# Performance work log

Measured on AMD Instinct MI355X. Metric: run time of the kernel, lower is better.

The kernel has to match this reference:

```python
import jax, jax.numpy as jnp
import numpy as np

B, T, I, H, OUT, L = 256, 1200, 16, 128, 1, 2


def _lstm_layer(x, W_ih, W_hh, b_ih, b_hh):
    # x: [B, T, Din]; W_ih: [4H, Din]; W_hh: [4H, H]
    # Precompute input contribution for all timesteps (one big GEMM),
    # then scan only the recurrent part.
    pre = jnp.einsum('btd,gd->btg', x, W_ih) + b_ih + b_hh  # [B, T, 4H]
    pre = jnp.swapaxes(pre, 0, 1)  # [T, B, 4H]
    h0 = jnp.zeros((x.shape[0], W_hh.shape[1]), dtype=x.dtype)
    c0 = jnp.zeros_like(h0)

    def step(carry, p_t):
        h, c = carry
        g = p_t + h @ W_hh.T  # [B, 4H]
        i, f, gg, o = jnp.split(g, 4, axis=-1)  # torch gate order: i, f, g, o
        i = jax.nn.sigmoid(i)
        f = jax.nn.sigmoid(f)
        gg = jnp.tanh(gg)
        o = jax.nn.sigmoid(o)
        c = f * c + i * gg
        h = o * jnp.tanh(c)
        return (h, c), h

    (_, _), hs = jax.lax.scan(step, (h0, c0), pre)  # hs: [T, B, H]
    return jnp.swapaxes(hs, 0, 1)  # [B, T, H]


def setup_inputs() -> dict:
    key = jax.random.key(0)
    ks = jax.random.split(key, 12)
    s = 0.08  # small init scale to keep gates unsaturated
    inp = {
        'x': jax.random.normal(ks[0], (B, T, I), dtype=jnp.float32),
        'W_ih0': jax.random.normal(ks[1], (4 * H, I), dtype=jnp.float32) * s,
        'W_hh0': jax.random.normal(ks[2], (4 * H, H), dtype=jnp.float32) * s,
        'b_ih0': jax.random.normal(ks[3], (4 * H,), dtype=jnp.float32) * s,
        'b_hh0': jax.random.normal(ks[4], (4 * H,), dtype=jnp.float32) * s,
        'W_ih1': jax.random.normal(ks[5], (4 * H, H), dtype=jnp.float32) * s,
        'W_hh1': jax.random.normal(ks[6], (4 * H, H), dtype=jnp.float32) * s,
        'b_ih1': jax.random.normal(ks[7], (4 * H,), dtype=jnp.float32) * s,
        'b_hh1': jax.random.normal(ks[8], (4 * H,), dtype=jnp.float32) * s,
        'W_lin': jax.random.normal(ks[9], (OUT, H), dtype=jnp.float32) * s,
        'b_lin': jax.random.normal(ks[10], (OUT,), dtype=jnp.float32) * s,
    }
    return inp


def reference(x, W_ih0, W_hh0, b_ih0, b_hh0, W_ih1, W_hh1, b_ih1, b_hh1, W_lin, b_lin):
    h1 = _lstm_layer(x, W_ih0, W_hh0, b_ih0, b_hh0)   # [B, T, H]
    h2 = _lstm_layer(h1, W_ih1, W_hh1, b_ih1, b_hh1)  # [B, T, H]
    out = jax.nn.relu(h2)
    out = jnp.einsum('bth,oh->bto', out, W_lin) + b_lin  # [B, T, OUT]
    return out.reshape(-1, 12)  # [B*T*OUT/12, 12]
```

## Files before the change

### kernel.cpp

```cpp
#include <hip/hip_runtime.h>
#include <hip/hip_fp16.h>

#define B_ 256
#define T_ 1200
#define I_ 16
#define H_ 128

typedef __attribute__((ext_vector_type(2))) _Float16 h2;
typedef __attribute__((ext_vector_type(8))) _Float16 f16x8;

union f16x8u { f16x8 v; h2 h[4]; };

#if __has_builtin(__builtin_amdgcn_fdot2)
__device__ __forceinline__ float fdot2(h2 a, h2 b, float c) {
  return __builtin_amdgcn_fdot2(a, b, c, false);
}
#else
__device__ __forceinline__ float fdot2(h2 a, h2 b, float c) {
  return fmaf((float)a.x, (float)b.x, fmaf((float)a.y, (float)b.y, c));
}
#endif

__device__ __forceinline__ float qsum(float x) {
  x += __int_as_float(__builtin_amdgcn_update_dpp(0, __float_as_int(x), 0xB1, 0xF, 0xF, true));
  x += __int_as_float(__builtin_amdgcn_update_dpp(0, __float_as_int(x), 0x4E, 0xF, 0xF, true));
  return x;
}

__device__ __forceinline__ float wred(float x) {
  x += __int_as_float(__builtin_amdgcn_update_dpp(0, __float_as_int(x), 0x141, 0xF, 0xF, true));
  x += __int_as_float(__builtin_amdgcn_update_dpp(0, __float_as_int(x), 0x140, 0xF, 0xF, true));
  x += __shfl_xor(x, 16);
  x += __shfl_xor(x, 32);
  return x;
}

__device__ __forceinline__ float sigm(float x) {
  return __builtin_amdgcn_rcpf(1.f + __expf(-x));
}
__device__ __forceinline__ float tanh_(float x) {
  return 1.f - 2.f * __builtin_amdgcn_rcpf(1.f + __expf(2.f * x));
}

__global__ __attribute__((amdgpu_waves_per_eu(2, 2)))
__launch_bounds__(512) void lstm_fused(
    const float* __restrict__ xin,
    const float* __restrict__ Wih0, const float* __restrict__ Whh0,
    const float* __restrict__ bih0, const float* __restrict__ bhh0,
    const float* __restrict__ Wih1, const float* __restrict__ Whh1,
    const float* __restrict__ bih1, const float* __restrict__ bhh1,
    const float* __restrict__ Wlin, const float* __restrict__ blin,
    float* __restrict__ out)
{
  __shared__ __align__(16) __half buf0[2][H_];
  __shared__ __align__(16) __half buf1[2][H_];
  __shared__ __align__(16) float red[2][8];

  const int tid = threadIdx.x;
  const int c = tid & 3;
  const int j = tid >> 2;
  const int b = blockIdx.x;
  const int wv = tid >> 6;

  h2 w0[4][16], wi[4][16], wh[4][16];
  h2 wx[4][2];
  float bs0[4], bs1[4];

#pragma unroll
  for (int q = 0; q < 4; ++q) {
    const int g = q * H_ + j;
    const float* p0 = Whh0 + (size_t)g * H_ + c * 32;
    const float* p1 = Wih1 + (size_t)g * H_ + c * 32;
    const float* p2 = Whh1 + (size_t)g * H_ + c * 32;
#pragma unroll
    for (int i = 0; i < 8; ++i) {
      float4 v = *(const float4*)(p0 + 4 * i);
      w0[q][2*i].x   = (_Float16)v.x; w0[q][2*i].y   = (_Float16)v.y;
      w0[q][2*i+1].x = (_Float16)v.z; w0[q][2*i+1].y = (_Float16)v.w;
      v = *(const float4*)(p1 + 4 * i);
      wi[q][2*i].x   = (_Float16)v.x; wi[q][2*i].y   = (_Float16)v.y;
      wi[q][2*i+1].x = (_Float16)v.z; wi[q][2*i+1].y = (_Float16)v.w;
      v = *(const float4*)(p2 + 4 * i);
      wh[q][2*i].x   = (_Float16)v.x; wh[q][2*i].y   = (_Float16)v.y;
      wh[q][2*i+1].x = (_Float16)v.z; wh[q][2*i+1].y = (_Float16)v.w;
    }
    const float4 vx = *(const float4*)(Wih0 + (size_t)g * I_ + 4 * c);
    wx[q][0].x = (_Float16)vx.x; wx[q][0].y = (_Float16)vx.y;
    wx[q][1].x = (_Float16)vx.z; wx[q][1].y = (_Float16)vx.w;
    bs0[q] = bih0[g] + bhh0[g];
    bs1[q] = bih1[g] + bhh1[g];
  }
  const float wl = Wlin[j];
  const float bl = blin[0];

  if (tid < H_) {
    buf0[0][tid] = __float2half(0.f);
    buf1[0][tid] = __float2half(0.f);
  }
  float cst0 = 0.f, cst1 = 0.f;
  const float* xp = xin + (size_t)b * T_ * I_ + 4 * c;
  float* op = out + (size_t)b * T_;
  __syncthreads();

#pragma unroll 2
  for (int t = 0; t < T_; ++t) {
    const int rb = t & 1;
    const float4 xv = *(const float4*)xp; xp += I_;
    float a0 = 0.f, a1 = 0.f, a2 = 0.f, a3 = 0.f;
#pragma unroll
    for (int i = 0; i < 4; ++i) {
      f16x8u u; u.v = *(const f16x8*)(&buf0[rb][c * 32 + i * 8]);
#pragma unroll
      for (int p = 0; p < 4; ++p) {
        const h2 hv = u.h[p];
        a0 = fdot2(w0[0][4 * i + p], hv, a0);
        a1 = fdot2(w0[1][4 * i + p], hv, a1);
        a2 = fdot2(w0[2][4 * i + p], hv, a2);
        a3 = fdot2(w0[3][4 * i + p], hv, a3);
      }
    }
    h2 xa, xb;
    xa.x = (_Float16)xv.x; xa.y = (_Float16)xv.y;
    xb.x = (_Float16)xv.z; xb.y = (_Float16)xv.w;
    a0 = fdot2(wx[0][0], xa, fdot2(wx[0][1], xb, a0));
    a1 = fdot2(wx[1][0], xa, fdot2(wx[1][1], xb, a1));
    a2 = fdot2(wx[2][0], xa, fdot2(wx[2][1], xb, a2));
    a3 = fdot2(wx[3][0], xa, fdot2(wx[3][1], xb, a3));
    {
      const float g0 = qsum(a0) + bs0[0];
      const float g1 = qsum(a1) + bs0[1];
      const float g2 = qsum(a2) + bs0[2];
      const float g3 = qsum(a3) + bs0[3];
      const float ig = sigm(g0), fg = sigm(g1), gg = tanh_(g2), og = sigm(g3);
      cst0 = fg * cst0 + ig * gg;
      const float h0v = og * tanh_(cst0);
      if (c == 0) buf0[rb ^ 1][j] = __float2half(h0v);
    }
    __syncthreads();
    a0 = 0.f; a1 = 0.f; a2 = 0.f; a3 = 0.f;
#pragma unroll
    for (int i = 0; i < 4; ++i) {
      f16x8u u; u.v = *(const f16x8*)(&buf0[rb ^ 1][c * 32 + i * 8]);
#pragma unroll
      for (int p = 0; p < 4; ++p) {
        const h2 hv = u.h[p];
        a0 = fdot2(wi[0][4 * i + p], hv, a0);
        a1 = fdot2(wi[1][4 * i + p], hv, a1);
        a2 = fdot2(wi[2][4 * i + p], hv, a2);
        a3 = fdot2(wi[3][4 * i + p], hv, a3);
      }
    }
#pragma unroll
    for (int i = 0; i < 4; ++i) {
      f16x8u u; u.v = *(const f16x8*)(&buf1[rb][c * 32 + i * 8]);
#pragma unroll
      for (int p = 0; p < 4; ++p) {
        const h2 hv = u.h[p];
        a0 = fdot2(wh[0][4 * i + p], hv, a0);
        a1 = fdot2(wh[1][4 * i + p], hv, a1);
        a2 = fdot2(wh[2][4 * i + p], hv, a2);
        a3 = fdot2(wh[3][4 * i + p], hv, a3);
      }
    }
    const float g0 = qsum(a0) + bs1[0];
    const float g1 = qsum(a1) + bs1[1];
    const float g2 = qsum(a2) + bs1[2];
    const float g3 = qsum(a3) + bs1[3];
    const float ig = sigm(g0), fg = sigm(g1), gg = tanh_(g2), og = sigm(g3);
    cst1 = fg * cst1 + ig * gg;
    const float h1v = og * tanh_(cst1);
    if (c == 0) buf1[rb ^ 1][j] = __float2half(h1v);
    float val = wred(fmaxf(h1v, 0.f) * wl);
    if ((tid & 63) == 0) red[rb][wv] = val;
    __syncthreads();
    if (tid == ((t & 7) << 6)) {
      const float4 r0 = *(const float4*)(&red[rb][0]);
      const float4 r1 = *(const float4*)(&red[rb][4]);
      op[t] = bl + r0.x + r0.y + r0.z + r0.w + r1.x + r1.y + r1.z + r1.w;
    }
  }
}

extern "C" void kernel_launch(void* const* d_in, const int* in_sizes, int n_in,
                              void* d_out, int out_size, void* d_ws, size_t ws_size,
                              hipStream_t stream) {
  lstm_fused<<<B_, 512, 0, stream>>>(
      (const float*)d_in[0],
      (const float*)d_in[1], (const float*)d_in[2],
      (const float*)d_in[3], (const float*)d_in[4],
      (const float*)d_in[5], (const float*)d_in[6],
      (const float*)d_in[7], (const float*)d_in[8],
      (const float*)d_in[9], (const float*)d_in[10],
      (float*)d_out);
}
```

Measured before the change: 1.752 ms.

## Split each hidden unit across 8 lanes with 1024-thread blocks

Doubles the block to 1024 threads so each hidden unit's dot products are split over 8 lanes instead of 4, which halves the per-thread serial fdot2 chain and the register-resident weights per step. The reductions are reworked to match the new lane split. Input weights and biases move from registers into shared memory and are reloaded every timestep, and the biases are stored as fp16. This shortens the per-step critical path in exchange for a deeper cross-lane reduction, more waves synchronising at each barrier, extra LDS traffic and slightly lower bias precision.

```diff
diff --git a/kernel.cpp b/kernel.cpp
--- a/kernel.cpp
+++ b/kernel.cpp
@@ -9,7 +9,7 @@
 typedef __attribute__((ext_vector_type(2))) _Float16 h2;
 typedef __attribute__((ext_vector_type(8))) _Float16 f16x8;
 
-union f16x8u { f16x8 v; h2 h[4]; };
+union f16x8u { f16x8 v; h2 h[4]; _Float16 s[8]; };
 
 #if __has_builtin(__builtin_amdgcn_fdot2)
 __device__ __forceinline__ float fdot2(h2 a, h2 b, float c) {
@@ -21,14 +21,14 @@
 }
 #endif
 
-__device__ __forceinline__ float qsum(float x) {
+__device__ __forceinline__ float qsum8(float x) {
   x += __int_as_float(__builtin_amdgcn_update_dpp(0, __float_as_int(x), 0xB1, 0xF, 0xF, true));
   x += __int_as_float(__builtin_amdgcn_update_dpp(0, __float_as_int(x), 0x4E, 0xF, 0xF, true));
+  x += __int_as_float(__builtin_amdgcn_update_dpp(0, __float_as_int(x), 0x141, 0xF, 0xF, true));
   return x;
 }
 
-__device__ __forceinline__ float wred(float x) {
-  x += __int_as_float(__builtin_amdgcn_update_dpp(0, __float_as_int(x), 0x141, 0xF, 0xF, true));
+__device__ __forceinline__ float ored(float x) {
   x += __int_as_float(__builtin_amdgcn_update_dpp(0, __float_as_int(x), 0x140, 0xF, 0xF, true));
   x += __shfl_xor(x, 16);
   x += __shfl_xor(x, 32);
@@ -42,8 +42,7 @@
   return 1.f - 2.f * __builtin_amdgcn_rcpf(1.f + __expf(2.f * x));
 }
 
-__global__ __attribute__((amdgpu_waves_per_eu(2, 2)))
-__launch_bounds__(512) void lstm_fused(
+__global__ __launch_bounds__(1024, 4) void lstm_fused(
     const float* __restrict__ xin,
     const float* __restrict__ Wih0, const float* __restrict__ Whh0,
     const float* __restrict__ bih0, const float* __restrict__ bhh0,
@@ -54,26 +53,26 @@
 {
   __shared__ __align__(16) __half buf0[2][H_];
   __shared__ __align__(16) __half buf1[2][H_];
-  __shared__ __align__(16) float red[2][8];
+  __shared__ __align__(16) float red[2][16];
+  __shared__ __align__(16) h2 lwx[128][8][4];
+  __shared__ __align__(16) __half lbh[128][8];
 
   const int tid = threadIdx.x;
-  const int c = tid & 3;
-  const int j = tid >> 2;
+  const int c = tid & 7;
+  const int j = tid >> 3;
   const int b = blockIdx.x;
   const int wv = tid >> 6;
 
-  h2 w0[4][16], wi[4][16], wh[4][16];
-  h2 wx[4][2];
-  float bs0[4], bs1[4];
+  h2 w0[4][8], wi[4][8], wh[4][8];
 
 #pragma unroll
   for (int q = 0; q < 4; ++q) {
     const int g = q * H_ + j;
-    const float* p0 = Whh0 + (size_t)g * H_ + c * 32;
-    const float* p1 = Wih1 + (size_t)g * H_ + c * 32;
-    const float* p2 = Whh1 + (size_t)g * H_ + c * 32;
-#pragma unroll
-    for (int i = 0; i < 8; ++i) {
+    const float* p0 = Whh0 + (size_t)g * H_ + c * 16;
+    const float* p1 = Wih1 + (size_t)g * H_ + c * 16;
+    const float* p2 = Whh1 + (size_t)g * H_ + c * 16;
+#pragma unroll
+    for (int i = 0; i < 4; ++i) {
       float4 v = *(const float4*)(p0 + 4 * i);
       w0[q][2*i].x   = (_Float16)v.x; w0[q][2*i].y   = (_Float16)v.y;
       w0[q][2*i+1].x = (_Float16)v.z; w0[q][2*i+1].y = (_Float16)v.w;
@@ -84,32 +83,37 @@
       wh[q][2*i].x   = (_Float16)v.x; wh[q][2*i].y   = (_Float16)v.y;
       wh[q][2*i+1].x = (_Float16)v.z; wh[q][2*i+1].y = (_Float16)v.w;
     }
-    const float4 vx = *(const float4*)(Wih0 + (size_t)g * I_ + 4 * c);
-    wx[q][0].x = (_Float16)vx.x; wx[q][0].y = (_Float16)vx.y;
-    wx[q][1].x = (_Float16)vx.z; wx[q][1].y = (_Float16)vx.w;
-    bs0[q] = bih0[g] + bhh0[g];
-    bs1[q] = bih1[g] + bhh1[g];
+    const float2 vx = *(const float2*)(Wih0 + (size_t)g * I_ + 2 * c);
+    h2 t; t.x = (_Float16)vx.x; t.y = (_Float16)vx.y;
+    lwx[j][c][q] = t;
+  }
+  if (tid < H_) {
+#pragma unroll
+    for (int q = 0; q < 4; ++q) {
+      const int g = q * H_ + tid;
+      lbh[tid][q]     = __float2half(bih0[g] + bhh0[g]);
+      lbh[tid][4 + q] = __float2half(bih1[g] + bhh1[g]);
+    }
+    buf0[0][tid] = __float2half(0.f);
+    buf1[0][tid] = __float2half(0.f);
   }
   const float wl = Wlin[j];
   const float bl = blin[0];
 
-  if (tid < H_) {
-    buf0[0][tid] = __float2half(0.f);
-    buf1[0][tid] = __float2half(0.f);
-  }
   float cst0 = 0.f, cst1 = 0.f;
-  const float* xp = xin + (size_t)b * T_ * I_ + 4 * c;
-  float* op = out + (size_t)b * T_;
+  const float* xp = xin + (size_t)b * T_ * I_ + 2 * c;
   __syncthreads();
 
-#pragma unroll 2
+#pragma unroll 1
   for (int t = 0; t < T_; ++t) {
     const int rb = t & 1;
-    const float4 xv = *(const float4*)xp; xp += I_;
+    const float2 xv = *(const float2*)xp; xp += I_;
+    f16x8u wxu; wxu.v = *(const f16x8*)(&lwx[j][c][0]);
+    f16x8u bu;  bu.v  = *(const f16x8*)(&lbh[j][0]);
     float a0 = 0.f, a1 = 0.f, a2 = 0.f, a3 = 0.f;
 #pragma unroll
-    for (int i = 0; i < 4; ++i) {
-      f16x8u u; u.v = *(const f16x8*)(&buf0[rb][c * 32 + i * 8]);
+    for (int i = 0; i < 2; ++i) {
+      f16x8u u; u.v = *(const f16x8*)(&buf0[rb][c * 16 + i * 8]);
 #pragma unroll
       for (int p = 0; p < 4; ++p) {
         const h2 hv = u.h[p];
@@ -119,18 +123,16 @@
         a3 = fdot2(w0[3][4 * i + p], hv, a3);
       }
     }
-    h2 xa, xb;
-    xa.x = (_Float16)xv.x; xa.y = (_Float16)xv.y;
-    xb.x = (_Float16)xv.z; xb.y = (_Float16)xv.w;
-    a0 = fdot2(wx[0][0], xa, fdot2(wx[0][1], xb, a0));
-    a1 = fdot2(wx[1][0], xa, fdot2(wx[1][1], xb, a1));
-    a2 = fdot2(wx[2][0], xa, fdot2(wx[2][1], xb, a2));
-    a3 = fdot2(wx[3][0], xa, fdot2(wx[3][1], xb, a3));
+    h2 xa; xa.x = (_Float16)xv.x; xa.y = (_Float16)xv.y;
+    a0 = fdot2(wxu.h[0], xa, a0);
+    a1 = fdot2(wxu.h[1], xa, a1);
+    a2 = fdot2(wxu.h[2], xa, a2);
+    a3 = fdot2(wxu.h[3], xa, a3);
     {
-      const float g0 = qsum(a0) + bs0[0];
-      const float g1 = qsum(a1) + bs0[1];
-      const float g2 = qsum(a2) + bs0[2];
-      const float g3 = qsum(a3) + bs0[3];
+      const float g0 = qsum8(a0) + (float)bu.s[0];
+      const float g1 = qsum8(a1) + (float)bu.s[1];
+      const float g2 = qsum8(a2) + (float)bu.s[2];
+      const float g3 = qsum8(a3) + (float)bu.s[3];
       const float ig = sigm(g0), fg = sigm(g1), gg = tanh_(g2), og = sigm(g3);
       cst0 = fg * cst0 + ig * gg;
       const float h0v = og * tanh_(cst0);
@@ -139,8 +141,8 @@
     __syncthreads();
     a0 = 0.f; a1 = 0.f; a2 = 0.f; a3 = 0.f;
 #pragma unroll
-    for (int i = 0; i < 4; ++i) {
-      f16x8u u; u.v = *(const f16x8*)(&buf0[rb ^ 1][c * 32 + i * 8]);
+    for (int i = 0; i < 2; ++i) {
+      f16x8u u; u.v = *(const f16x8*)(&buf0[rb ^ 1][c * 16 + i * 8]);
 #pragma unroll
       for (int p = 0; p < 4; ++p) {
         const h2 hv = u.h[p];
@@ -151,8 +153,8 @@
       }
     }
 #pragma unroll
-    for (int i = 0; i < 4; ++i) {
-      f16x8u u; u.v = *(const f16x8*)(&buf1[rb][c * 32 + i * 8]);
+    for (int i = 0; i < 2; ++i) {
+      f16x8u u; u.v = *(const f16x8*)(&buf1[rb][c * 16 + i * 8]);
 #pragma unroll
       for (int p = 0; p < 4; ++p) {
         const h2 hv = u.h[p];
@@ -162,21 +164,25 @@
         a3 = fdot2(wh[3][4 * i + p], hv, a3);
       }
     }
-    const float g0 = qsum(a0) + bs1[0];
-    const float g1 = qsum(a1) + bs1[1];
-    const float g2 = qsum(a2) + bs1[2];
-    const float g3 = qsum(a3) + bs1[3];
+    const float g0 = qsum8(a0) + (float)bu.s[4];
+    const float g1 = qsum8(a1) + (float)bu.s[5];
+    const float g2 = qsum8(a2) + (float)bu.s[6];
+    const float g3 = qsum8(a3) + (float)bu.s[7];
     const float ig = sigm(g0), fg = sigm(g1), gg = tanh_(g2), og = sigm(g3);
     cst1 = fg * cst1 + ig * gg;
     const float h1v = og * tanh_(cst1);
     if (c == 0) buf1[rb ^ 1][j] = __float2half(h1v);
-    float val = wred(fmaxf(h1v, 0.f) * wl);
+    float val = ored(fmaxf(h1v, 0.f) * wl);
     if ((tid & 63) == 0) red[rb][wv] = val;
     __syncthreads();
-    if (tid == ((t & 7) << 6)) {
+    if (tid == ((t & 15) << 6)) {
       const float4 r0 = *(const float4*)(&red[rb][0]);
       const float4 r1 = *(const float4*)(&red[rb][4]);
-      op[t] = bl + r0.x + r0.y + r0.z + r0.w + r1.x + r1.y + r1.z + r1.w;
+      const float4 r2 = *(const float4*)(&red[rb][8]);
+      const float4 r3 = *(const float4*)(&red[rb][12]);
+      out[(size_t)b * T_ + t] = bl
+          + r0.x + r0.y + r0.z + r0.w + r1.x + r1.y + r1.z + r1.w
+          + r2.x + r2.y + r2.z + r2.w + r3.x + r3.y + r3.z + r3.w;
     }
   }
 }
@@ -184,7 +190,7 @@
 extern "C" void kernel_launch(void* const* d_in, const int* in_sizes, int n_in,
                               void* d_out, int out_size, void* d_ws, size_t ws_size,
                               hipStream_t stream) {
-  lstm_fused<<<B_, 512, 0, stream>>>(
+  lstm_fused<<<B_, 1024, 0, stream>>>(
       (const float*)d_in[0],
       (const float*)d_in[1], (const float*)d_in[2],
       (const float*)d_in[3], (const float*)d_in[4],
```

After: 2.704 ms. 1.54x slower.

## Split fused two-layer LSTM into layer0, input-projection GEMM, and layer1 kernels

Applied to the files above, without the earlier changes.

Replaces the single fused kernel with three launches when workspace is large enough. Layer 0 runs its recurrence with x staged in LDS and writes h0 to workspace as fp16. A separate kernel computes the layer-1 input projection for all timesteps. Layer 1 then runs only its recurrent matvec plus the precomputed term. Each thread now owns one full gate row with a broadcast instead of a 4-way reduction, which shortens the per-step serial chain. The cost is about 400 MB of extra global traffic, a serialized second recurrence, and more fp16 rounding in the intermediates.

```diff
diff --git a/kernel.cpp b/kernel.cpp
--- a/kernel.cpp
+++ b/kernel.cpp
@@ -5,11 +5,12 @@
 #define T_ 1200
 #define I_ 16
 #define H_ 128
+#define G4_ (4 * H_)
 
 typedef __attribute__((ext_vector_type(2))) _Float16 h2;
 typedef __attribute__((ext_vector_type(8))) _Float16 f16x8;
 
-union f16x8u { f16x8 v; h2 h[4]; };
+union f16x8u { f16x8 v; h2 h[4]; _Float16 s[8]; };
 
 #if __has_builtin(__builtin_amdgcn_fdot2)
 __device__ __forceinline__ float fdot2(h2 a, h2 b, float c) {
@@ -21,10 +22,9 @@
 }
 #endif
 
-__device__ __forceinline__ float qsum(float x) {
-  x += __int_as_float(__builtin_amdgcn_update_dpp(0, __float_as_int(x), 0xB1, 0xF, 0xF, true));
-  x += __int_as_float(__builtin_amdgcn_update_dpp(0, __float_as_int(x), 0x4E, 0xF, 0xF, true));
-  return x;
+template <int PAT>
+__device__ __forceinline__ float qbcast(float x) {
+  return __int_as_float(__builtin_amdgcn_update_dpp(0, __float_as_int(x), PAT, 0xF, 0xF, true));
 }
 
 __device__ __forceinline__ float wred(float x) {
@@ -42,8 +42,197 @@
   return 1.f - 2.f * __builtin_amdgcn_rcpf(1.f + __expf(2.f * x));
 }
 
-__global__ __attribute__((amdgpu_waves_per_eu(2, 2)))
-__launch_bounds__(512) void lstm_fused(
+__device__ __forceinline__ void load_row_h2(const float* __restrict__ p, h2* w) {
+#pragma unroll
+  for (int i = 0; i < 32; ++i) {
+    const float4 v = *(const float4*)(p + 4 * i);
+    w[2 * i].x     = (_Float16)v.x; w[2 * i].y     = (_Float16)v.y;
+    w[2 * i + 1].x = (_Float16)v.z; w[2 * i + 1].y = (_Float16)v.w;
+  }
+}
+
+__global__ __launch_bounds__(512, 2) void k1_layer0(
+    const float* __restrict__ xin,
+    const float* __restrict__ Wih0, const float* __restrict__ Whh0,
+    const float* __restrict__ bih0, const float* __restrict__ bhh0,
+    __half* __restrict__ h0ws)
+{
+  __shared__ __align__(16) __half xs[T_ * I_];
+  __shared__ __align__(16) __half hb[2][H_];
+
+  const int tid = threadIdx.x;
+  const int q = tid & 3;
+  const int j = tid >> 2;
+  const int g = q * H_ + j;
+  const int b = blockIdx.x;
+
+  {
+    const float4* xg4 = (const float4*)(xin + (size_t)b * T_ * I_);
+    for (int idx = tid; idx < T_ * I_ / 4; idx += 512) {
+      const float4 v = xg4[idx];
+      xs[4 * idx]     = __float2half(v.x);
+      xs[4 * idx + 1] = __float2half(v.y);
+      xs[4 * idx + 2] = __float2half(v.z);
+      xs[4 * idx + 3] = __float2half(v.w);
+    }
+  }
+
+  h2 wh[64], wx[8];
+  load_row_h2(Whh0 + (size_t)g * H_, wh);
+  {
+    const float* px = Wih0 + (size_t)g * I_;
+#pragma unroll
+    for (int i = 0; i < 4; ++i) {
+      const float4 v = *(const float4*)(px + 4 * i);
+      wx[2 * i].x     = (_Float16)v.x; wx[2 * i].y     = (_Float16)v.y;
+      wx[2 * i + 1].x = (_Float16)v.z; wx[2 * i + 1].y = (_Float16)v.w;
+    }
+  }
+  const float bs = bih0[g] + bhh0[g];
+
+  if (tid < H_) hb[0][tid] = __float2half(0.f);
+  float cst = 0.f;
+  __half* h0o = h0ws + (size_t)b * T_ * H_ + j;
+  __syncthreads();
+
+#pragma unroll 2
+  for (int t = 0; t < T_; ++t) {
+    const int rb = t & 1;
+    float a0 = 0.f, a1 = 0.f, a2 = 0.f, a3 = 0.f;
+#pragma unroll
+    for (int i = 0; i < 16; ++i) {
+      f16x8u u; u.v = *(const f16x8*)(&hb[rb][8 * i]);
+      a0 = fdot2(wh[4 * i],     u.h[0], a0);
+      a1 = fdot2(wh[4 * i + 1], u.h[1], a1);
+      a2 = fdot2(wh[4 * i + 2], u.h[2], a2);
+      a3 = fdot2(wh[4 * i + 3], u.h[3], a3);
+    }
+#pragma unroll
+    for (int m = 0; m < 2; ++m) {
+      f16x8u u; u.v = *(const f16x8*)(&xs[t * I_ + 8 * m]);
+      a0 = fdot2(wx[4 * m],     u.h[0], a0);
+      a1 = fdot2(wx[4 * m + 1], u.h[1], a1);
+      a2 = fdot2(wx[4 * m + 2], u.h[2], a2);
+      a3 = fdot2(wx[4 * m + 3], u.h[3], a3);
+    }
+    const float pre = (a0 + a1) + (a2 + a3) + bs;
+    const float ip = qbcast<0x00>(pre);
+    const float fp = qbcast<0x55>(pre);
+    const float gp = qbcast<0xAA>(pre);
+    const float op = qbcast<0xFF>(pre);
+    const float ig = sigm(ip), fg = sigm(fp), gg = tanh_(gp), og = sigm(op);
+    cst = fg * cst + ig * gg;
+    const float hv = og * tanh_(cst);
+    const __half hh = __float2half(hv);
+    if (q == 0) {
+      hb[rb ^ 1][j] = hh;
+      h0o[(size_t)t * H_] = hh;
+    }
+    __syncthreads();
+  }
+}
+
+__global__ __launch_bounds__(512, 2) void k2_pregemm(
+    const __half* __restrict__ h0ws,
+    const float* __restrict__ Wih1,
+    __half* __restrict__ pre1)
+{
+  const int g = threadIdx.x;
+  const int b = blockIdx.x;
+
+  h2 w[64];
+  load_row_h2(Wih1 + (size_t)g * H_, w);
+
+  const __half* hrow = h0ws + (size_t)b * T_ * H_;
+  __half* pp = pre1 + (size_t)b * T_ * G4_ + g;
+
+#pragma unroll 2
+  for (int t = 0; t < T_; ++t) {
+    const __half* hr = hrow + (size_t)t * H_;
+    float a0 = 0.f, a1 = 0.f, a2 = 0.f, a3 = 0.f;
+#pragma unroll
+    for (int i = 0; i < 16; ++i) {
+      f16x8u u; u.v = *(const f16x8*)(hr + 8 * i);
+      a0 = fdot2(w[4 * i],     u.h[0], a0);
+      a1 = fdot2(w[4 * i + 1], u.h[1], a1);
+      a2 = fdot2(w[4 * i + 2], u.h[2], a2);
+      a3 = fdot2(w[4 * i + 3], u.h[3], a3);
+    }
+    pp[(size_t)t * G4_] = __float2half((a0 + a1) + (a2 + a3));
+  }
+}
+
+__global__ __launch_bounds__(512, 2) void k3_layer1(
+    const __half* __restrict__ pre1,
+    const float* __restrict__ Whh1,
+    const float* __restrict__ bih1, const float* __restrict__ bhh1,
+    const float* __restrict__ Wlin, const float* __restrict__ blin,
+    float* __restrict__ out)
+{
+  __shared__ __align__(16) __half hb[2][H_];
+  __shared__ __align__(16) float red[2][8];
+
+  const int tid = threadIdx.x;
+  const int q = tid & 3;
+  const int j = tid >> 2;
+  const int g = q * H_ + j;
+  const int b = blockIdx.x;
+  const int wv = tid >> 6;
+
+  h2 w[64];
+  load_row_h2(Whh1 + (size_t)g * H_, w);
+  const float bs = bih1[g] + bhh1[g];
+  const float wl = Wlin[j];
+  const float bl = blin[0];
+
+  if (tid < H_) hb[0][tid] = __float2half(0.f);
+  float cst = 0.f;
+  const __half* pp = pre1 + (size_t)b * T_ * G4_ + g;
+  float* op = out + (size_t)b * T_;
+  __syncthreads();
+
+  __half pnext = pp[0];
+#pragma unroll 2
+  for (int t = 0; t < T_; ++t) {
+    const int rb = t & 1;
+    const __half pcur = pnext;
+    if (t + 1 < T_) pnext = pp[(size_t)(t + 1) * G4_];
+    float a0 = 0.f, a1 = 0.f, a2 = 0.f, a3 = 0.f;
+#pragma unroll
+    for (int i = 0; i < 16; ++i) {
+      f16x8u u; u.v = *(const f16x8*)(&hb[rb][8 * i]);
+      a0 = fdot2(w[4 * i],     u.h[0], a0);
+      a1 = fdot2(w[4 * i + 1], u.h[1], a1);
+      a2 = fdot2(w[4 * i + 2], u.h[2], a2);
+      a3 = fdot2(w[4 * i + 3], u.h[3], a3);
+    }
+    const float pre = (a0 + a1) + (a2 + a3) + __half2float(pcur) + bs;
+    const float ip = qbcast<0x00>(pre);
+    const float fp = qbcast<0x55>(pre);
+    const float gp = qbcast<0xAA>(pre);
+    const float op_ = qbcast<0xFF>(pre);
+    const float ig = sigm(ip), fg = sigm(fp), gg = tanh_(gp), og = sigm(op_);
+    cst = fg * cst + ig * gg;
+    const float hv = og * tanh_(cst);
+    if (q == 0) hb[rb ^ 1][j] = __float2half(hv);
+    float val = wred(fmaxf(hv, 0.f) * wl);
+    if ((tid & 63) == 0) red[rb][wv] = val;
+    __syncthreads();
+    if (tid == ((t & 7) << 6)) {
+      const float4 r0 = *(const float4*)(&red[rb][0]);
+      const float4 r1 = *(const float4*)(&red[rb][4]);
+      op[t] = bl + r0.x + r0.y + r0.z + r0.w + r1.x + r1.y + r1.z + r1.w;
+    }
+  }
+}
+
+__device__ __forceinline__ float qsum8f(float x) {
+  x += __int_as_float(__builtin_amdgcn_update_dpp(0, __float_as_int(x), 0xB1, 0xF, 0xF, true));
+  x += __int_as_float(__builtin_amdgcn_update_dpp(0, __float_as_int(x), 0x4E, 0xF, 0xF, true));
+  return x;
+}
+
+__global__ __launch_bounds__(512, 2) void lstm_fused_fb(
     const float* __restrict__ xin,
     const float* __restrict__ Wih0, const float* __restrict__ Whh0,
     const float* __restrict__ bih0, const float* __restrict__ bhh0,
@@ -67,28 +256,28 @@
   float bs0[4], bs1[4];
 
 #pragma unroll
-  for (int q = 0; q < 4; ++q) {
-    const int g = q * H_ + j;
+  for (int qq = 0; qq < 4; ++qq) {
+    const int g = qq * H_ + j;
     const float* p0 = Whh0 + (size_t)g * H_ + c * 32;
     const float* p1 = Wih1 + (size_t)g * H_ + c * 32;
     const float* p2 = Whh1 + (size_t)g * H_ + c * 32;
 #pragma unroll
     for (int i = 0; i < 8; ++i) {
       float4 v = *(const float4*)(p0 + 4 * i);
-      w0[q][2*i].x   = (_Float16)v.x; w0[q][2*i].y   = (_Float16)v.y;
-      w0[q][2*i+1].x = (_Float16)v.z; w0[q][2*i+1].y = (_Float16)v.w;
+      w0[qq][2*i].x   = (_Float16)v.x; w0[qq][2*i].y   = (_Float16)v.y;
+      w0[qq][2*i+1].x = (_Float16)v.z; w0[qq][2*i+1].y = (_Float16)v.w;
       v = *(const float4*)(p1 + 4 * i);
-      wi[q][2*i].x   = (_Float16)v.x; wi[q][2*i].y   = (_Float16)v.y;
-      wi[q][2*i+1].x = (_Float16)v.z; wi[q][2*i+1].y = (_Float16)v.w;
+      wi[qq][2*i].x   = (_Float16)v.x; wi[qq][2*i].y   = (_Float16)v.y;
+      wi[qq][2*i+1].x = (_Float16)v.z; wi[qq][2*i+1].y = (_Float16)v.w;
       v = *(const float4*)(p2 + 4 * i);
-      wh[q][2*i].x   = (_Float16)v.x; wh[q][2*i].y   = (_Float16)v.y;
-      wh[q][2*i+1].x = (_Float16)v.z; wh[q][2*i+1].y = (_Float16)v.w;
+      wh[qq][2*i].x   = (_Float16)v.x; wh[qq][2*i].y   = (_Float16)v.y;
+      wh[qq][2*i+1].x = (_Float16)v.z; wh[qq][2*i+1].y = (_Float16)v.w;
     }
     const float4 vx = *(const float4*)(Wih0 + (size_t)g * I_ + 4 * c);
-    wx[q][0].x = (_Float16)vx.x; wx[q][0].y = (_Float16)vx.y;
-    wx[q][1].x = (_Float16)vx.z; wx[q][1].y = (_Float16)vx.w;
-    bs0[q] = bih0[g] + bhh0[g];
-    bs1[q] = bih1[g] + bhh1[g];
+    wx[qq][0].x = (_Float16)vx.x; wx[qq][0].y = (_Float16)vx.y;
+    wx[qq][1].x = (_Float16)vx.z; wx[qq][1].y = (_Float16)vx.w;
+    bs0[qq] = bih0[g] + bhh0[g];
+    bs1[qq] = bih1[g] + bhh1[g];
   }
   const float wl = Wlin[j];
   const float bl = blin[0];
@@ -127,10 +316,10 @@
     a2 = fdot2(wx[2][0], xa, fdot2(wx[2][1], xb, a2));
     a3 = fdot2(wx[3][0], xa, fdot2(wx[3][1], xb, a3));
     {
-      const float g0 = qsum(a0) + bs0[0];
-      const float g1 = qsum(a1) + bs0[1];
-      const float g2 = qsum(a2) + bs0[2];
-      const float g3 = qsum(a3) + bs0[3];
+      const float g0 = qsum8f(a0) + bs0[0];
+      const float g1 = qsum8f(a1) + bs0[1];
+      const float g2 = qsum8f(a2) + bs0[2];
+      const float g3 = qsum8f(a3) + bs0[3];
       const float ig = sigm(g0), fg = sigm(g1), gg = tanh_(g2), og = sigm(g3);
       cst0 = fg * cst0 + ig * gg;
       const float h0v = og * tanh_(cst0);
@@ -162,10 +351,10 @@
         a3 = fdot2(wh[3][4 * i + p], hv, a3);
       }
     }
-    const float g0 = qsum(a0) + bs1[0];
-    const float g1 = qsum(a1) + bs1[1];
-    const float g2 = qsum(a2) + bs1[2];
-    const float g3 = qsum(a3) + bs1[3];
+    const float g0 = qsum8f(a0) + bs1[0];
+    const float g1 = qsum8f(a1) + bs1[1];
+    const float g2 = qsum8f(a2) + bs1[2];
+    const float g3 = qsum8f(a3) + bs1[3];
     const float ig = sigm(g0), fg = sigm(g1), gg = tanh_(g2), og = sigm(g3);
     cst1 = fg * cst1 + ig * gg;
     const float h1v = og * tanh_(cst1);
@@ -184,12 +373,32 @@
 extern "C" void kernel_launch(void* const* d_in, const int* in_sizes, int n_in,
                               void* d_out, int out_size, void* d_ws, size_t ws_size,
                               hipStream_t stream) {
-  lstm_fused<<<B_, 512, 0, stream>>>(
-      (const float*)d_in[0],
-      (const float*)d_in[1], (const float*)d_in[2],
-      (const float*)d_in[3], (const float*)d_in[4],
-      (const float*)d_in[5], (const float*)d_in[6],
-      (const float*)d_in[7], (const float*)d_in[8],
-      (const float*)d_in[9], (const float*)d_in[10],
-      (float*)d_out);
-}
+  const size_t H0_BYTES  = (size_t)B_ * T_ * H_ * sizeof(__half);
+  const size_t PRE_BYTES = (size_t)B_ * T_ * G4_ * sizeof(__half);
+
+  if (d_ws != nullptr && ws_size >= H0_BYTES + PRE_BYTES) {
+    __half* h0ws = (__half*)d_ws;
+    __half* pre1 = (__half*)((char*)d_ws + H0_BYTES);
+    k1_layer0<<<B_, 512, 0, stream>>>(
+        (const float*)d_in[0],
+        (const float*)d_in[1], (const float*)d_in[2],
+        (const float*)d_in[3], (const float*)d_in[4],
+        h0ws);
+    k2_pregemm<<<B_, 512, 0, stream>>>(
+        h0ws, (const float*)d_in[5], pre1);
+    k3_layer1<<<B_, 512, 0, stream>>>(
+        pre1, (const float*)d_in[6],
+        (const float*)d_in[7], (const float*)d_in[8],
+        (const float*)d_in[9], (const float*)d_in[10],
+        (float*)d_out);
+  } else {
+    lstm_fused_fb<<<B_, 512, 0, stream>>>(
+        (const float*)d_in[0],
+        (const float*)d_in[1], (const float*)d_in[2],
+        (const float*)d_in[3], (const float*)d_in[4],
+        (const float*)d_in[5], (const float*)d_in[6],
+        (const float*)d_in[7], (const float*)d_in[8],
+        (const float*)d_in[9], (const float*)d_in[10],
+        (float*)d_out);
+  }
+}
```

New measurement: 1.751 ms. Within noise of the previous version (-0.1%).

## Pipeline LSTM layers across timesteps with one barrier per step and per-thread gate rows

Applied to the files above, without the earlier changes.

Layer 1 for step t-1 now runs in the same iteration as layer 0 for step t, which cuts the block barriers from two per step to one. Each thread owns a full gate row, so the cross-lane reductions are replaced by one unified sigmoid/tanh activation per lane and DPP broadcasts of the four gates. The input sequence is staged into LDS as fp16 up front, and the output reduction is deferred by a step. In exchange, each thread holds about 200 half2 weight registers, which risks register pressure or spills. Every thread also reads the whole h vector from LDS, which raises LDS traffic.

```diff
diff --git a/kernel.cpp b/kernel.cpp
--- a/kernel.cpp
+++ b/kernel.cpp
@@ -9,7 +9,7 @@
 typedef __attribute__((ext_vector_type(2))) _Float16 h2;
 typedef __attribute__((ext_vector_type(8))) _Float16 f16x8;
 
-union f16x8u { f16x8 v; h2 h[4]; };
+union f16x8u { f16x8 v; h2 h[4]; _Float16 s[8]; };
 
 #if __has_builtin(__builtin_amdgcn_fdot2)
 __device__ __forceinline__ float fdot2(h2 a, h2 b, float c) {
@@ -21,10 +21,9 @@
 }
 #endif
 
-__device__ __forceinline__ float qsum(float x) {
-  x += __int_as_float(__builtin_amdgcn_update_dpp(0, __float_as_int(x), 0xB1, 0xF, 0xF, true));
-  x += __int_as_float(__builtin_amdgcn_update_dpp(0, __float_as_int(x), 0x4E, 0xF, 0xF, true));
-  return x;
+template <int PAT>
+__device__ __forceinline__ float qbcast(float x) {
+  return __int_as_float(__builtin_amdgcn_update_dpp(0, __float_as_int(x), PAT, 0xF, 0xF, true));
 }
 
 __device__ __forceinline__ float wred(float x) {
@@ -35,15 +34,27 @@
   return x;
 }
 
-__device__ __forceinline__ float sigm(float x) {
-  return __builtin_amdgcn_rcpf(1.f + __expf(-x));
-}
 __device__ __forceinline__ float tanh_(float x) {
   return 1.f - 2.f * __builtin_amdgcn_rcpf(1.f + __expf(2.f * x));
 }
 
-__global__ __attribute__((amdgpu_waves_per_eu(2, 2)))
-__launch_bounds__(512) void lstm_fused(
+__device__ __forceinline__ void load_row_h2(const float* __restrict__ p, h2* w) {
+#pragma unroll
+  for (int i = 0; i < 32; ++i) {
+    const float4 v = *(const float4*)(p + 4 * i);
+    w[2 * i].x     = (_Float16)v.x; w[2 * i].y     = (_Float16)v.y;
+    w[2 * i + 1].x = (_Float16)v.z; w[2 * i + 1].y = (_Float16)v.w;
+  }
+}
+
+__device__ __forceinline__ void lds_barrier() {
+  __builtin_amdgcn_sched_barrier(0);
+  asm volatile("s_waitcnt lgkmcnt(0)" ::: "memory");
+  __builtin_amdgcn_s_barrier();
+  __builtin_amdgcn_sched_barrier(0);
+}
+
+__global__ __launch_bounds__(512, 2) void lstm_one(
     const float* __restrict__ xin,
     const float* __restrict__ Wih0, const float* __restrict__ Whh0,
     const float* __restrict__ bih0, const float* __restrict__ bhh0,
@@ -52,139 +63,151 @@
     const float* __restrict__ Wlin, const float* __restrict__ blin,
     float* __restrict__ out)
 {
-  __shared__ __align__(16) __half buf0[2][H_];
-  __shared__ __align__(16) __half buf1[2][H_];
+  __shared__ __align__(16) __half xs[T_ * I_];
+  __shared__ __align__(16) __half h0b[2][H_];
+  __shared__ __align__(16) __half h1b[2][H_];
   __shared__ __align__(16) float red[2][8];
 
   const int tid = threadIdx.x;
-  const int c = tid & 3;
+  const int q = tid & 3;
   const int j = tid >> 2;
+  const int g = q * H_ + j;
   const int b = blockIdx.x;
-  const int wv = tid >> 6;
-
-  h2 w0[4][16], wi[4][16], wh[4][16];
-  h2 wx[4][2];
-  float bs0[4], bs1[4];
-
-#pragma unroll
-  for (int q = 0; q < 4; ++q) {
-    const int g = q * H_ + j;
-    const float* p0 = Whh0 + (size_t)g * H_ + c * 32;
-    const float* p1 = Wih1 + (size_t)g * H_ + c * 32;
-    const float* p2 = Whh1 + (size_t)g * H_ + c * 32;
-#pragma unroll
-    for (int i = 0; i < 8; ++i) {
-      float4 v = *(const float4*)(p0 + 4 * i);
-      w0[q][2*i].x   = (_Float16)v.x; w0[q][2*i].y   = (_Float16)v.y;
-      w0[q][2*i+1].x = (_Float16)v.z; w0[q][2*i+1].y = (_Float16)v.w;
-      v = *(const float4*)(p1 + 4 * i);
-      wi[q][2*i].x   = (_Float16)v.x; wi[q][2*i].y   = (_Float16)v.y;
-      wi[q][2*i+1].x = (_Float16)v.z; wi[q][2*i+1].y = (_Float16)v.w;
-      v = *(const float4*)(p2 + 4 * i);
-      wh[q][2*i].x   = (_Float16)v.x; wh[q][2*i].y   = (_Float16)v.y;
-      wh[q][2*i+1].x = (_Float16)v.z; wh[q][2*i+1].y = (_Float16)v.w;
-    }
-    const float4 vx = *(const float4*)(Wih0 + (size_t)g * I_ + 4 * c);
-    wx[q][0].x = (_Float16)vx.x; wx[q][0].y = (_Float16)vx.y;
-    wx[q][1].x = (_Float16)vx.z; wx[q][1].y = (_Float16)vx.w;
-    bs0[q] = bih0[g] + bhh0[g];
-    bs1[q] = bih1[g] + bhh1[g];
-  }
+
+  {
+    const float4* xg4 = (const float4*)(xin + (size_t)b * T_ * I_);
+    for (int idx = tid; idx < T_ * I_ / 4; idx += 512) {
+      const float4 v = xg4[idx];
+      xs[4 * idx]     = __float2half(v.x);
+      xs[4 * idx + 1] = __float2half(v.y);
+      xs[4 * idx + 2] = __float2half(v.z);
+      xs[4 * idx + 3] = __float2half(v.w);
+    }
+  }
+
+  h2 w0[64], wi[64], w1[64], wx[8];
+  load_row_h2(Whh0 + (size_t)g * H_, w0);
+  load_row_h2(Wih1 + (size_t)g * H_, wi);
+  load_row_h2(Whh1 + (size_t)g * H_, w1);
+  {
+    const float* px = Wih0 + (size_t)g * I_;
+#pragma unroll
+    for (int i = 0; i < 4; ++i) {
+      const float4 v = *(const float4*)(px + 4 * i);
+      wx[2 * i].x     = (_Float16)v.x; wx[2 * i].y     = (_Float16)v.y;
+      wx[2 * i + 1].x = (_Float16)v.z; wx[2 * i + 1].y = (_Float16)v.w;
+    }
+  }
+  const float bs0 = bih0[g] + bhh0[g];
+  const float bs1 = bih1[g] + bhh1[g];
   const float wl = Wlin[j];
   const float bl = blin[0];
+  const float s0 = (q == 2) ? 1.f : 0.f;
+  const float s1 = (q == 2) ? -2.f : 1.f;
+  const float s2 = (q == 2) ? 2.f : -1.f;
 
   if (tid < H_) {
-    buf0[0][tid] = __float2half(0.f);
-    buf1[0][tid] = __float2half(0.f);
-  }
-  float cst0 = 0.f, cst1 = 0.f;
-  const float* xp = xin + (size_t)b * T_ * I_ + 4 * c;
+    h0b[0][tid] = __float2half(0.f);
+    h1b[0][tid] = __float2half(0.f);
+    h1b[1][tid] = __float2half(0.f);
+  }
+  float cst0 = 0.f, cst1 = 0.f, hv1p = 0.f;
   float* op = out + (size_t)b * T_;
   __syncthreads();
 
-#pragma unroll 2
-  for (int t = 0; t < T_; ++t) {
-    const int rb = t & 1;
-    const float4 xv = *(const float4*)xp; xp += I_;
-    float a0 = 0.f, a1 = 0.f, a2 = 0.f, a3 = 0.f;
-#pragma unroll
-    for (int i = 0; i < 4; ++i) {
-      f16x8u u; u.v = *(const f16x8*)(&buf0[rb][c * 32 + i * 8]);
-#pragma unroll
-      for (int p = 0; p < 4; ++p) {
-        const h2 hv = u.h[p];
-        a0 = fdot2(w0[0][4 * i + p], hv, a0);
-        a1 = fdot2(w0[1][4 * i + p], hv, a1);
-        a2 = fdot2(w0[2][4 * i + p], hv, a2);
-        a3 = fdot2(w0[3][4 * i + p], hv, a3);
-      }
-    }
-    h2 xa, xb;
-    xa.x = (_Float16)xv.x; xa.y = (_Float16)xv.y;
-    xb.x = (_Float16)xv.z; xb.y = (_Float16)xv.w;
-    a0 = fdot2(wx[0][0], xa, fdot2(wx[0][1], xb, a0));
-    a1 = fdot2(wx[1][0], xa, fdot2(wx[1][1], xb, a1));
-    a2 = fdot2(wx[2][0], xa, fdot2(wx[2][1], xb, a2));
-    a3 = fdot2(wx[3][0], xa, fdot2(wx[3][1], xb, a3));
-    {
-      const float g0 = qsum(a0) + bs0[0];
-      const float g1 = qsum(a1) + bs0[1];
-      const float g2 = qsum(a2) + bs0[2];
-      const float g3 = qsum(a3) + bs0[3];
-      const float ig = sigm(g0), fg = sigm(g1), gg = tanh_(g2), og = sigm(g3);
+#pragma unroll 1
+  for (int u = 0; u <= T_ + 2; ++u) {
+    const int rb = u & 1, nb = rb ^ 1;
+
+    if (u >= 2 && u <= T_ + 1) {
+      const float val = wred(fmaxf(hv1p, 0.f) * wl);
+      if ((tid & 63) == 0) red[rb][tid >> 6] = val;
+    }
+    if (u >= 3) {
+      const int m = u - 3;
+      if (tid == ((m & 7) << 6)) {
+        const float4 r0 = *(const float4*)(&red[nb][0]);
+        const float4 r1 = *(const float4*)(&red[nb][4]);
+        op[m] = bl + r0.x + r0.y + r0.z + r0.w + r1.x + r1.y + r1.z + r1.w;
+      }
+    }
+
+    float A0 = 0.f, A1 = 0.f, A2 = 0.f, A3 = 0.f;
+    float B0 = 0.f, B1 = 0.f, B2 = 0.f, B3 = 0.f;
+    float C0 = 0.f, C1 = 0.f, C2 = 0.f, C3 = 0.f;
+
+    if (u >= 1 && u < T_) {
+#pragma unroll
+      for (int i = 0; i < 16; ++i) {
+        f16x8u u8; u8.v = *(const f16x8*)(&h0b[rb][8 * i]);
+        A0 = fdot2(w0[4 * i],     u8.h[0], A0);
+        A1 = fdot2(w0[4 * i + 1], u8.h[1], A1);
+        A2 = fdot2(w0[4 * i + 2], u8.h[2], A2);
+        A3 = fdot2(w0[4 * i + 3], u8.h[3], A3);
+        B0 = fdot2(wi[4 * i],     u8.h[0], B0);
+        B1 = fdot2(wi[4 * i + 1], u8.h[1], B1);
+        B2 = fdot2(wi[4 * i + 2], u8.h[2], B2);
+        B3 = fdot2(wi[4 * i + 3], u8.h[3], B3);
+      }
+    } else if (u == T_) {
+#pragma unroll
+      for (int i = 0; i < 16; ++i) {
+        f16x8u u8; u8.v = *(const f16x8*)(&h0b[rb][8 * i]);
+        B0 = fdot2(wi[4 * i],     u8.h[0], B0);
+        B1 = fdot2(wi[4 * i + 1], u8.h[1], B1);
+        B2 = fdot2(wi[4 * i + 2], u8.h[2], B2);
+        B3 = fdot2(wi[4 * i + 3], u8.h[3], B3);
+      }
+    }
+
+    if (u < T_) {
+#pragma unroll
+      for (int m2 = 0; m2 < 2; ++m2) {
+        f16x8u u8; u8.v = *(const f16x8*)(&xs[u * I_ + 8 * m2]);
+        A0 = fdot2(wx[4 * m2],     u8.h[0], A0);
+        A1 = fdot2(wx[4 * m2 + 1], u8.h[1], A1);
+        A2 = fdot2(wx[4 * m2 + 2], u8.h[2], A2);
+        A3 = fdot2(wx[4 * m2 + 3], u8.h[3], A3);
+      }
+      const float pre = (A0 + A1) + (A2 + A3) + bs0;
+      const float act = fmaf(s1, __builtin_amdgcn_rcpf(1.f + __expf(s2 * pre)), s0);
+      const float ig = qbcast<0x00>(act);
+      const float fg = qbcast<0x55>(act);
+      const float gg = qbcast<0xAA>(act);
+      const float og = qbcast<0xFF>(act);
       cst0 = fg * cst0 + ig * gg;
-      const float h0v = og * tanh_(cst0);
-      if (c == 0) buf0[rb ^ 1][j] = __float2half(h0v);
-    }
-    __syncthreads();
-    a0 = 0.f; a1 = 0.f; a2 = 0.f; a3 = 0.f;
-#pragma unroll
-    for (int i = 0; i < 4; ++i) {
-      f16x8u u; u.v = *(const f16x8*)(&buf0[rb ^ 1][c * 32 + i * 8]);
-#pragma unroll
-      for (int p = 0; p < 4; ++p) {
-        const h2 hv = u.h[p];
-        a0 = fdot2(wi[0][4 * i + p], hv, a0);
-        a1 = fdot2(wi[1][4 * i + p], hv, a1);
-        a2 = fdot2(wi[2][4 * i + p], hv, a2);
-        a3 = fdot2(wi[3][4 * i + p], hv, a3);
-      }
-    }
-#pragma unroll
-    for (int i = 0; i < 4; ++i) {
-      f16x8u u; u.v = *(const f16x8*)(&buf1[rb][c * 32 + i * 8]);
-#pragma unroll
-      for (int p = 0; p < 4; ++p) {
-        const h2 hv = u.h[p];
-        a0 = fdot2(wh[0][4 * i + p], hv, a0);
-        a1 = fdot2(wh[1][4 * i + p], hv, a1);
-        a2 = fdot2(wh[2][4 * i + p], hv, a2);
-        a3 = fdot2(wh[3][4 * i + p], hv, a3);
-      }
-    }
-    const float g0 = qsum(a0) + bs1[0];
-    const float g1 = qsum(a1) + bs1[1];
-    const float g2 = qsum(a2) + bs1[2];
-    const float g3 = qsum(a3) + bs1[3];
-    const float ig = sigm(g0), fg = sigm(g1), gg = tanh_(g2), og = sigm(g3);
-    cst1 = fg * cst1 + ig * gg;
-    const float h1v = og * tanh_(cst1);
-    if (c == 0) buf1[rb ^ 1][j] = __float2half(h1v);
-    float val = wred(fmaxf(h1v, 0.f) * wl);
-    if ((tid & 63) == 0) red[rb][wv] = val;
-    __syncthreads();
-    if (tid == ((t & 7) << 6)) {
-      const float4 r0 = *(const float4*)(&red[rb][0]);
-      const float4 r1 = *(const float4*)(&red[rb][4]);
-      op[t] = bl + r0.x + r0.y + r0.z + r0.w + r1.x + r1.y + r1.z + r1.w;
-    }
+      const float hv0 = og * tanh_(cst0);
+      if (q == 0) h0b[nb][j] = __float2half(hv0);
+    }
+
+    if (u >= 1 && u <= T_) {
+#pragma unroll
+      for (int i = 0; i < 16; ++i) {
+        f16x8u u8; u8.v = *(const f16x8*)(&h1b[rb][8 * i]);
+        C0 = fdot2(w1[4 * i],     u8.h[0], C0);
+        C1 = fdot2(w1[4 * i + 1], u8.h[1], C1);
+        C2 = fdot2(w1[4 * i + 2], u8.h[2], C2);
+        C3 = fdot2(w1[4 * i + 3], u8.h[3], C3);
+      }
+      const float pre = (B0 + B1) + (B2 + B3) + (C0 + C1) + (C2 + C3) + bs1;
+      const float act = fmaf(s1, __builtin_amdgcn_rcpf(1.f + __expf(s2 * pre)), s0);
+      const float ig = qbcast<0x00>(act);
+      const float fg = qbcast<0x55>(act);
+      const float gg = qbcast<0xAA>(act);
+      const float og = qbcast<0xFF>(act);
+      cst1 = fg * cst1 + ig * gg;
+      hv1p = og * tanh_(cst1);
+      if (q == 0) h1b[nb][j] = __float2half(hv1p);
+    }
+
+    if (u <= T_ + 1) lds_barrier();
   }
 }
 
 extern "C" void kernel_launch(void* const* d_in, const int* in_sizes, int n_in,
                               void* d_out, int out_size, void* d_ws, size_t ws_size,
                               hipStream_t stream) {
-  lstm_fused<<<B_, 512, 0, stream>>>(
+  lstm_one<<<B_, 512, 0, stream>>>(
       (const float*)d_in[0],
       (const float*)d_in[1], (const float*)d_in[2],
       (const float*)d_in[3], (const float*)d_in[4],
```

Result: slower. 1.933 ms (+10.3%).
